# Optimization experiments

Measured on AMD Instinct MI355X. Metric: run time of the kernel, lower is better.

## Reference

```python
import jax, jax.numpy as jnp
import numpy as np

# Inner-product factors for Cl(1,3) (Minkowski metric diag(+,-,-,-)).
# For blade e_b, <~e_b e_b>_0 = product of the metric signs of its constituent vectors.
# Blade order: [1, e0,e1,e2,e3, e01,e02,e03,e12,e13,e23, e012,e013,e023,e123, e0123]
_IPF = jnp.array([1, 1, -1, -1, -1, -1, -1, -1, 1, 1, 1, 1, 1, 1, -1, -1], dtype=jnp.float32)

B, H, N, CMV, CS = 4, 8, 2048, 8, 16


def setup_inputs() -> dict:
    key = jax.random.key(0)
    ks = jax.random.split(key, 6)
    f = lambda k, s: jax.random.normal(k, s, dtype=jnp.float32)
    return {
        "q_mv": f(ks[0], (B, H, N, CMV, 16)),
        "k_mv": f(ks[1], (B, H, N, CMV, 16)),
        "v_mv": f(ks[2], (B, H, N, CMV, 16)),
        "q_s": f(ks[3], (B, H, N, CS)),
        "k_s": f(ks[4], (B, H, N, CS)),
        "v_s": f(ks[5], (B, H, N, CS)),
    }


def reference(q_mv, k_mv, v_mv, q_s, k_s, v_s):
    b, h, n, cmv, _ = q_mv.shape
    cs = q_s.shape[-1]
    cmv_out = v_mv.shape[-2]
    cs_out = v_s.shape[-1]
    # GA inner product on mv part = euclidean dot after applying metric factors to queries
    q = jnp.concatenate([(q_mv * _IPF).reshape(b, h, n, cmv * 16), q_s], axis=-1)
    k = jnp.concatenate([k_mv.reshape(b, h, n, cmv * 16), k_s], axis=-1)
    v = jnp.concatenate([v_mv.reshape(b, h, n, cmv_out * 16), v_s], axis=-1)
    scale = 1.0 / np.sqrt(q.shape[-1]).astype(np.float32)  # torch SDPA default scale
    scores = jnp.einsum("bhid,bhjd->bhij", q, k) * scale  # [B,H,N,N]
    attn = jax.nn.softmax(scores, axis=-1)
    out = jnp.einsum("bhij,bhjd->bhid", attn, v)
    out_mv = out[..., : cmv_out * 16].reshape(b, h, n, cmv_out, 16)
    out_s = out[..., cmv_out * 16 : cmv_out * 16 + cs_out]
    return out_mv, out_s
```

## Files before the change

### kernel.cpp

```cpp
#include <hip/hip_runtime.h>
#include <cstdint>
#include <math.h>


#define BH    32
#define N_    2048
#define DMV   128
#define DS    16
#define D_    144
#define BM    128
#define BN    64
#define NKIT  (N_ / BN)
#define KSTR  168
#define VSTR  72
#define PSTR  72
#define KP_BYTES  ((size_t)BH * N_ * KSTR * 2)
#define QSCALE 0.12022458674074693f

typedef __bf16 bf16_8 __attribute__((ext_vector_type(8)));
typedef __bf16 bf16_4 __attribute__((ext_vector_type(4)));
typedef __bf16 bf16_2 __attribute__((ext_vector_type(2)));
typedef float  f32x4  __attribute__((ext_vector_type(4)));

#define GLOAD_LDS16(g, l)                                                     \
  __builtin_amdgcn_global_load_lds(                                           \
      (const __attribute__((address_space(1))) void*)(g),                     \
      (__attribute__((address_space(3))) void*)(l), 16, 0, 0)

__device__ __forceinline__ f32x4 mfma16(bf16_8 a, bf16_8 b, f32x4 c) {
  return __builtin_amdgcn_mfma_f32_16x16x32_bf16(a, b, c, 0, 0, 0);
}

__device__ __forceinline__ bf16_4 cvt4(f32x4 x) {
  bf16_4 w; w[0]=(__bf16)x[0]; w[1]=(__bf16)x[1]; w[2]=(__bf16)x[2]; w[3]=(__bf16)x[3];
  return w;
}

__global__ __launch_bounds__(256)
void pack_k(const float* __restrict__ kmv, const float* __restrict__ ks_,
            __bf16* __restrict__ kp) {
  const unsigned g = blockIdx.x * 256 + threadIdx.x;
  const unsigned row = g / 21u, seg = g - row * 21u;
  bf16_8 o;
  if (seg < 16) {
    const f32x4* p = (const f32x4*)(kmv + (size_t)row * DMV + seg * 8);
    f32x4 a = p[0], b = p[1];
#pragma unroll
    for (int j = 0; j < 8; ++j) o[j] = (__bf16)((j < 4) ? a[j] : b[j - 4]);
  } else if (seg < 18) {
    const f32x4* p = (const f32x4*)(ks_ + (size_t)row * DS + (seg - 16) * 8);
    f32x4 a = p[0], b = p[1];
#pragma unroll
    for (int j = 0; j < 8; ++j) o[j] = (__bf16)((j < 4) ? a[j] : b[j - 4]);
  } else {
#pragma unroll
    for (int j = 0; j < 8; ++j) o[j] = (__bf16)0.0f;
  }
  *(bf16_8*)(kp + (size_t)row * KSTR + seg * 8) = o;
}

#define TSTR 156
__global__ __launch_bounds__(256)
void pack_vt(const float* __restrict__ vmv, const float* __restrict__ vs,
             __bf16* __restrict__ vt) {
  __shared__ __bf16 sT[64 * TSTR];
  const int tile = blockIdx.x;
  const int t = threadIdx.x;
  const int n = t >> 2, c = t & 3;
  const float* mv = vmv + (size_t)(tile * 64 + n) * DMV;
  const float* s  = vs  + (size_t)(tile * 64 + n) * DS;
  __bf16* row = &sT[n * TSTR];
  if (c < 3) {
#pragma unroll
    for (int i = 0; i < 9; ++i)
      *(bf16_4*)&row[c * 36 + 4 * i] = cvt4(*(const f32x4*)(mv + c * 36 + 4 * i));
  } else {
#pragma unroll
    for (int i = 0; i < 5; ++i)
      *(bf16_4*)&row[108 + 4 * i] = cvt4(*(const f32x4*)(mv + 108 + 4 * i));
#pragma unroll
    for (int i = 0; i < 4; ++i)
      *(bf16_4*)&row[128 + 4 * i] = cvt4(*(const f32x4*)(s + 4 * i));
  }
  __syncthreads();
  __bf16* vtt = vt + (size_t)tile * (D_ * VSTR);
#pragma unroll
  for (int k = 0; k < 18; ++k) {
    int idx = t + 256 * k;
    int d = idx >> 5, j = idx & 31;
    bf16_2 p; p[0] = sT[(2 * j) * TSTR + d]; p[1] = sT[(2 * j + 1) * TSTR + d];
    *(bf16_2*)&vtt[d * VSTR + 2 * j] = p;
  }
}

__device__ __forceinline__ bf16_8 load_q_frag(const float* qmv_row, const float* qs_row, int k0) {
  bf16_8 f;
  if (k0 < DMV) {
    const f32x4* p = (const f32x4*)(qmv_row + k0);
    f32x4 a = p[0], b = p[1];
    int hi = k0 & 8;
#pragma unroll
    for (int j = 0; j < 8; ++j) {
      float v = (j < 4) ? a[j] : b[j - 4];
      bool pos = hi ? (j < 6) : (j < 2);
      f[j] = (__bf16)(v * (pos ? QSCALE : -QSCALE));
    }
  } else if (k0 < D_) {
    const f32x4* p = (const f32x4*)(qs_row + (k0 - DMV));
    f32x4 a = p[0], b = p[1];
#pragma unroll
    for (int j = 0; j < 8; ++j) {
      float v = (j < 4) ? a[j] : b[j - 4];
      f[j] = (__bf16)(v * QSCALE);
    }
  } else {
#pragma unroll
    for (int j = 0; j < 8; ++j) f[j] = (__bf16)0.0f;
  }
  return f;
}

__global__ __launch_bounds__(512, 4)
void geo_attn_kernel(const float* __restrict__ q_mv, const float* __restrict__ q_s,
                     const __bf16* __restrict__ kp, const __bf16* __restrict__ vt,
                     float* __restrict__ out)
{
  __shared__ __bf16 sK[BN * KSTR];
  __shared__ __bf16 sVT[D_ * VSTR];

  const int tid  = threadIdx.x;
  const int w    = tid >> 6;
  const int lane = tid & 63;
  const int l15  = lane & 15;
  const int quad = lane >> 4;
  const int bh    = blockIdx.y;
  const int qbase = blockIdx.x * BM;
  const size_t bh_n = (size_t)bh * N_;

  __bf16* sP = sK + w * (16 * PSTR);

  bf16_8 qf[5];
  {
    int mrow = qbase + 16 * w + l15;
    const float* qmv_row = q_mv + (bh_n + mrow) * DMV;
    const float* qs_row  = q_s  + (bh_n + mrow) * DS;
#pragma unroll
    for (int ks = 0; ks < 5; ++ks)
      qf[ks] = load_q_frag(qmv_row, qs_row, ks * 32 + quad * 8);
  }

  f32x4 of[9];
#pragma unroll
  for (int n9 = 0; n9 < 9; ++n9)
#pragma unroll
    for (int r = 0; r < 4; ++r) of[n9][r] = 0.0f;
  float m_i = -INFINITY, l_i = 0.0f;

  const __bf16* kbase = kp + bh_n * KSTR;

  for (int it = 0; it < NKIT; ++it) {
    {
      const __bf16* kt  = kbase + (size_t)(it * BN) * KSTR;
      const __bf16* vtt = vt + (size_t)(bh * NKIT + it) * (D_ * VSTR);
      for (int i = w; i < 21; i += 8)
        GLOAD_LDS16(kt + i * 512 + lane * 8, &sK[i * 512 + lane * 8]);
      for (int i = w; i < 20; i += 8)
        GLOAD_LDS16(vtt + i * 512 + lane * 8, &sVT[i * 512 + lane * 8]);
      if (w == 0 && lane < 16)
        GLOAD_LDS16(vtt + 20 * 512 + lane * 8, &sVT[20 * 512 + lane * 8]);
    }
    __syncthreads();

    f32x4 sf[4];
#pragma unroll
    for (int nt = 0; nt < 4; ++nt)
#pragma unroll
      for (int r = 0; r < 4; ++r) sf[nt][r] = 0.0f;
#pragma unroll
    for (int ks = 0; ks < 5; ++ks) {
#pragma unroll
      for (int nt = 0; nt < 4; ++nt) {
        bf16_8 kb = *(const bf16_8*)&sK[(nt * 16 + l15) * KSTR + ks * 32 + quad * 8];
        sf[nt] = mfma16(kb, qf[ks], sf[nt]);
      }
    }
    __syncthreads();

    {
      float mx = sf[0][0];
#pragma unroll
      for (int nt = 0; nt < 4; ++nt)
#pragma unroll
        for (int r = 0; r < 4; ++r) mx = fmaxf(mx, sf[nt][r]);
      mx = fmaxf(mx, __shfl_xor(mx, 16));
      mx = fmaxf(mx, __shfl_xor(mx, 32));
      float mnew = fmaxf(m_i, mx);
      float al = __builtin_amdgcn_exp2f(m_i - mnew);
      m_i = mnew;
      float rs = 0.0f;
#pragma unroll
      for (int nt = 0; nt < 4; ++nt)
#pragma unroll
        for (int r = 0; r < 4; ++r) {
          float p = __builtin_amdgcn_exp2f(sf[nt][r] - mnew);
          sf[nt][r] = p;
          rs += p;
        }
      rs += __shfl_xor(rs, 16);
      rs += __shfl_xor(rs, 32);
      l_i = l_i * al + rs;

#pragma unroll
      for (int nt = 0; nt < 4; ++nt) {
        bf16_4 pw;
#pragma unroll
        for (int r = 0; r < 4; ++r) pw[r] = (__bf16)sf[nt][r];
        *(bf16_4*)&sP[l15 * PSTR + nt * 16 + quad * 4] = pw;
      }
      asm volatile("s_waitcnt lgkmcnt(0)" ::: "memory");

      float alr[4];
#pragma unroll
      for (int r = 0; r < 4; ++r) alr[r] = __shfl(al, 20 * quad + r);
#pragma unroll
      for (int n9 = 0; n9 < 9; ++n9)
#pragma unroll
        for (int r = 0; r < 4; ++r) of[n9][r] *= alr[r];
    }

#pragma unroll
    for (int ks = 0; ks < 2; ++ks) {
      bf16_8 pa = *(const bf16_8*)&sP[l15 * PSTR + ks * 32 + quad * 8];
#pragma unroll
      for (int n9 = 0; n9 < 9; ++n9) {
        bf16_8 vb = *(const bf16_8*)&sVT[(n9 * 16 + l15) * VSTR + ks * 32 + quad * 8];
        of[n9] = mfma16(pa, vb, of[n9]);
      }
    }
    __syncthreads();
  }

  float* out_mv = out;
  float* out_s  = out + (size_t)BH * N_ * DMV;
  float linv[4];
#pragma unroll
  for (int r = 0; r < 4; ++r)
    linv[r] = __builtin_amdgcn_rcpf(__shfl(l_i, 20 * quad + r));
#pragma unroll
  for (int n9 = 0; n9 < 9; ++n9) {
#pragma unroll
    for (int r = 0; r < 4; ++r) {
      int row = qbase + 16 * w + quad * 4 + r;
      float val = of[n9][r] * linv[r];
      if (n9 < 8) out_mv[(bh_n + row) * DMV + n9 * 16 + l15] = val;
      else        out_s [(bh_n + row) * DS + l15] = val;
    }
  }
}

extern "C" void kernel_launch(void* const* d_in, const int* in_sizes, int n_in,
                              void* d_out, int out_size, void* d_ws, size_t ws_size,
                              hipStream_t stream) {
  (void)in_sizes; (void)n_in; (void)out_size; (void)ws_size;
  const float* q_mv = (const float*)d_in[0];
  const float* k_mv = (const float*)d_in[1];
  const float* v_mv = (const float*)d_in[2];
  const float* q_s  = (const float*)d_in[3];
  const float* k_s  = (const float*)d_in[4];
  const float* v_s  = (const float*)d_in[5];
  float* out = (float*)d_out;

  __bf16* kp = (__bf16*)d_ws;
  __bf16* vt = (__bf16*)((char*)d_ws + KP_BYTES);

  pack_k<<<(BH * N_ * 21) / 256, 256, 0, stream>>>(k_mv, k_s, kp);
  pack_vt<<<BH * NKIT, 256, 0, stream>>>(v_mv, v_s, vt);

  dim3 grid(N_ / BM, BH);
  geo_attn_kernel<<<grid, 512, 0, stream>>>(q_mv, q_s, kp, vt, out);
}
```

Measured before the change: 273.6 us.

## Pre-swizzle K/V tiles into MFMA fragment order and give each wave two row groups

The pack kernels now write K and V^T tiles in the exact per-lane MFMA fragment order, so LDS reads become contiguous lane*8 accesses with no padding strides. The attention kernel drops from 8 waves to 4 per block, and each wave handles 32 query rows as two 16-row groups. Every K and V fragment loaded from LDS is then reused for two MFMAs. This cuts LDS traffic and bank conflicts per MFMA, but it doubles accumulator registers per wave and lowers wave count per block, which may hurt occupancy and latency hiding.

```diff
diff --git a/kernel.cpp b/kernel.cpp
--- a/kernel.cpp
+++ b/kernel.cpp
@@ -11,15 +11,13 @@
 #define BM    128
 #define BN    64
 #define NKIT  (N_ / BN)
-#define KSTR  168
-#define VSTR  72
 #define PSTR  72
-#define KP_BYTES  ((size_t)BH * N_ * KSTR * 2)
+#define KTILE_E  10240
+#define VTILE_E  9216
+#define KP_BYTES ((size_t)BH * NKIT * KTILE_E * 2)
 #define QSCALE 0.12022458674074693f
 
 typedef __bf16 bf16_8 __attribute__((ext_vector_type(8)));
-typedef __bf16 bf16_4 __attribute__((ext_vector_type(4)));
-typedef __bf16 bf16_2 __attribute__((ext_vector_type(2)));
 typedef float  f32x4  __attribute__((ext_vector_type(4)));
 
 #define GLOAD_LDS16(g, l)                                                     \
@@ -31,32 +29,37 @@
   return __builtin_amdgcn_mfma_f32_16x16x32_bf16(a, b, c, 0, 0, 0);
 }
 
-__device__ __forceinline__ bf16_4 cvt4(f32x4 x) {
-  bf16_4 w; w[0]=(__bf16)x[0]; w[1]=(__bf16)x[1]; w[2]=(__bf16)x[2]; w[3]=(__bf16)x[3];
-  return w;
-}
-
 __global__ __launch_bounds__(256)
 void pack_k(const float* __restrict__ kmv, const float* __restrict__ ks_,
             __bf16* __restrict__ kp) {
-  const unsigned g = blockIdx.x * 256 + threadIdx.x;
-  const unsigned row = g / 21u, seg = g - row * 21u;
-  bf16_8 o;
-  if (seg < 16) {
-    const f32x4* p = (const f32x4*)(kmv + (size_t)row * DMV + seg * 8);
-    f32x4 a = p[0], b = p[1];
-#pragma unroll
-    for (int j = 0; j < 8; ++j) o[j] = (__bf16)((j < 4) ? a[j] : b[j - 4]);
-  } else if (seg < 18) {
-    const f32x4* p = (const f32x4*)(ks_ + (size_t)row * DS + (seg - 16) * 8);
-    f32x4 a = p[0], b = p[1];
-#pragma unroll
-    for (int j = 0; j < 8; ++j) o[j] = (__bf16)((j < 4) ? a[j] : b[j - 4]);
-  } else {
-#pragma unroll
-    for (int j = 0; j < 8; ++j) o[j] = (__bf16)0.0f;
-  }
-  *(bf16_8*)(kp + (size_t)row * KSTR + seg * 8) = o;
+  const int tile = blockIdx.x;
+  const int t = threadIdx.x;
+  __bf16* dst = kp + (size_t)tile * KTILE_E;
+#pragma unroll
+  for (int u = 0; u < 5; ++u) {
+    int c = t + 256 * u;
+    int f = c >> 6, r = c & 63;
+    int nt = f / 5, ks = f - nt * 5;
+    int quad = r >> 4, l15 = r & 15;
+    int n = tile * 64 + nt * 16 + l15;
+    int k = ks * 32 + quad * 8;
+    bf16_8 o;
+    if (k < DMV) {
+      const f32x4* p = (const f32x4*)(kmv + (size_t)n * DMV + k);
+      f32x4 a = p[0], b = p[1];
+#pragma unroll
+      for (int j = 0; j < 8; ++j) o[j] = (__bf16)((j < 4) ? a[j] : b[j - 4]);
+    } else if (k < D_) {
+      const f32x4* p = (const f32x4*)(ks_ + (size_t)n * DS + (k - DMV));
+      f32x4 a = p[0], b = p[1];
+#pragma unroll
+      for (int j = 0; j < 8; ++j) o[j] = (__bf16)((j < 4) ? a[j] : b[j - 4]);
+    } else {
+#pragma unroll
+      for (int j = 0; j < 8; ++j) o[j] = (__bf16)0.0f;
+    }
+    *(bf16_8*)(dst + (size_t)c * 8) = o;
+  }
 }
 
 #define TSTR 156
@@ -66,30 +69,45 @@
   __shared__ __bf16 sT[64 * TSTR];
   const int tile = blockIdx.x;
   const int t = threadIdx.x;
-  const int n = t >> 2, c = t & 3;
-  const float* mv = vmv + (size_t)(tile * 64 + n) * DMV;
-  const float* s  = vs  + (size_t)(tile * 64 + n) * DS;
-  __bf16* row = &sT[n * TSTR];
-  if (c < 3) {
-#pragma unroll
-    for (int i = 0; i < 9; ++i)
-      *(bf16_4*)&row[c * 36 + 4 * i] = cvt4(*(const f32x4*)(mv + c * 36 + 4 * i));
-  } else {
-#pragma unroll
-    for (int i = 0; i < 5; ++i)
-      *(bf16_4*)&row[108 + 4 * i] = cvt4(*(const f32x4*)(mv + 108 + 4 * i));
-#pragma unroll
-    for (int i = 0; i < 4; ++i)
-      *(bf16_4*)&row[128 + 4 * i] = cvt4(*(const f32x4*)(s + 4 * i));
+  {
+    const int n = t >> 2, c4 = t & 3;
+    const float* mv = vmv + (size_t)(tile * 64 + n) * DMV;
+    const float* s  = vs  + (size_t)(tile * 64 + n) * DS;
+    __bf16* row = &sT[n * TSTR];
+    if (c4 < 3) {
+#pragma unroll
+      for (int i = 0; i < 9; ++i) {
+        f32x4 x = *(const f32x4*)(mv + c4 * 36 + 4 * i);
+#pragma unroll
+        for (int j = 0; j < 4; ++j) row[c4 * 36 + 4 * i + j] = (__bf16)x[j];
+      }
+    } else {
+#pragma unroll
+      for (int i = 0; i < 5; ++i) {
+        f32x4 x = *(const f32x4*)(mv + 108 + 4 * i);
+#pragma unroll
+        for (int j = 0; j < 4; ++j) row[108 + 4 * i + j] = (__bf16)x[j];
+      }
+#pragma unroll
+      for (int i = 0; i < 4; ++i) {
+        f32x4 x = *(const f32x4*)(s + 4 * i);
+#pragma unroll
+        for (int j = 0; j < 4; ++j) row[128 + 4 * i + j] = (__bf16)x[j];
+      }
+    }
   }
   __syncthreads();
-  __bf16* vtt = vt + (size_t)tile * (D_ * VSTR);
-#pragma unroll
-  for (int k = 0; k < 18; ++k) {
-    int idx = t + 256 * k;
-    int d = idx >> 5, j = idx & 31;
-    bf16_2 p; p[0] = sT[(2 * j) * TSTR + d]; p[1] = sT[(2 * j + 1) * TSTR + d];
-    *(bf16_2*)&vtt[d * VSTR + 2 * j] = p;
+  __bf16* dst = vt + (size_t)tile * VTILE_E;
+  for (int c = t; c < 1152; c += 256) {
+    int f = c >> 6, r = c & 63;
+    int n9 = f >> 1, ks = f & 1;
+    int quad = r >> 4, l15 = r & 15;
+    int d = n9 * 16 + l15;
+    int n0 = ks * 32 + quad * 8;
+    bf16_8 o;
+#pragma unroll
+    for (int j = 0; j < 8; ++j) o[j] = sT[(n0 + j) * TSTR + d];
+    *(bf16_8*)(dst + (size_t)c * 8) = o;
   }
 }
 
@@ -120,13 +138,13 @@
   return f;
 }
 
-__global__ __launch_bounds__(512, 4)
+__global__ __launch_bounds__(256, 3)
 void geo_attn_kernel(const float* __restrict__ q_mv, const float* __restrict__ q_s,
                      const __bf16* __restrict__ kp, const __bf16* __restrict__ vt,
                      float* __restrict__ out)
 {
-  __shared__ __bf16 sK[BN * KSTR];
-  __shared__ __bf16 sVT[D_ * VSTR];
+  __shared__ __bf16 sK[KTILE_E];
+  __shared__ __bf16 sVT[VTILE_E];
 
   const int tid  = threadIdx.x;
   const int w    = tid >> 6;
@@ -137,87 +155,92 @@
   const int qbase = blockIdx.x * BM;
   const size_t bh_n = (size_t)bh * N_;
 
-  __bf16* sP = sK + w * (16 * PSTR);
-
-  bf16_8 qf[5];
-  {
-    int mrow = qbase + 16 * w + l15;
+  __bf16* sPw = sK + w * (32 * PSTR);
+
+  bf16_8 qf[2][5];
+#pragma unroll
+  for (int rg = 0; rg < 2; ++rg) {
+    int mrow = qbase + 32 * w + 16 * rg + l15;
     const float* qmv_row = q_mv + (bh_n + mrow) * DMV;
     const float* qs_row  = q_s  + (bh_n + mrow) * DS;
 #pragma unroll
     for (int ks = 0; ks < 5; ++ks)
-      qf[ks] = load_q_frag(qmv_row, qs_row, ks * 32 + quad * 8);
-  }
-
-  f32x4 of[9];
-#pragma unroll
-  for (int n9 = 0; n9 < 9; ++n9)
-#pragma unroll
-    for (int r = 0; r < 4; ++r) of[n9][r] = 0.0f;
-  float m_i = -INFINITY, l_i = 0.0f;
-
-  const __bf16* kbase = kp + bh_n * KSTR;
+      qf[rg][ks] = load_q_frag(qmv_row, qs_row, ks * 32 + quad * 8);
+  }
+
+  f32x4 of[2][9];
+#pragma unroll
+  for (int rg = 0; rg < 2; ++rg)
+#pragma unroll
+    for (int n9 = 0; n9 < 9; ++n9)
+#pragma unroll
+      for (int r = 0; r < 4; ++r) of[rg][n9][r] = 0.0f;
+  float m_i[2] = {-INFINITY, -INFINITY}, l_i[2] = {0.0f, 0.0f};
+
+  const __bf16* kbase = kp + (size_t)bh * NKIT * KTILE_E;
+  const __bf16* vbase = vt + (size_t)bh * NKIT * VTILE_E;
 
   for (int it = 0; it < NKIT; ++it) {
     {
-      const __bf16* kt  = kbase + (size_t)(it * BN) * KSTR;
-      const __bf16* vtt = vt + (size_t)(bh * NKIT + it) * (D_ * VSTR);
-      for (int i = w; i < 21; i += 8)
+      const __bf16* kt = kbase + (size_t)it * KTILE_E;
+      const __bf16* vp = vbase + (size_t)it * VTILE_E;
+      for (int i = w; i < 20; i += 4)
         GLOAD_LDS16(kt + i * 512 + lane * 8, &sK[i * 512 + lane * 8]);
-      for (int i = w; i < 20; i += 8)
-        GLOAD_LDS16(vtt + i * 512 + lane * 8, &sVT[i * 512 + lane * 8]);
-      if (w == 0 && lane < 16)
-        GLOAD_LDS16(vtt + 20 * 512 + lane * 8, &sVT[20 * 512 + lane * 8]);
+      for (int i = w; i < 18; i += 4)
+        GLOAD_LDS16(vp + i * 512 + lane * 8, &sVT[i * 512 + lane * 8]);
     }
     __syncthreads();
 
-    f32x4 sf[4];
-#pragma unroll
-    for (int nt = 0; nt < 4; ++nt)
-#pragma unroll
-      for (int r = 0; r < 4; ++r) sf[nt][r] = 0.0f;
+    f32x4 sf[2][4];
+#pragma unroll
+    for (int rg = 0; rg < 2; ++rg)
+#pragma unroll
+      for (int nt = 0; nt < 4; ++nt)
+#pragma unroll
+        for (int r = 0; r < 4; ++r) sf[rg][nt][r] = 0.0f;
 #pragma unroll
     for (int ks = 0; ks < 5; ++ks) {
 #pragma unroll
       for (int nt = 0; nt < 4; ++nt) {
-        bf16_8 kb = *(const bf16_8*)&sK[(nt * 16 + l15) * KSTR + ks * 32 + quad * 8];
-        sf[nt] = mfma16(kb, qf[ks], sf[nt]);
+        bf16_8 kb = *(const bf16_8*)&sK[(nt * 5 + ks) * 512 + lane * 8];
+        sf[0][nt] = mfma16(kb, qf[0][ks], sf[0][nt]);
+        sf[1][nt] = mfma16(kb, qf[1][ks], sf[1][nt]);
       }
     }
     __syncthreads();
 
-    {
-      float mx = sf[0][0];
+#pragma unroll
+    for (int rg = 0; rg < 2; ++rg) {
+      float mx = sf[rg][0][0];
 #pragma unroll
       for (int nt = 0; nt < 4; ++nt)
 #pragma unroll
-        for (int r = 0; r < 4; ++r) mx = fmaxf(mx, sf[nt][r]);
+        for (int r = 0; r < 4; ++r) mx = fmaxf(mx, sf[rg][nt][r]);
       mx = fmaxf(mx, __shfl_xor(mx, 16));
       mx = fmaxf(mx, __shfl_xor(mx, 32));
-      float mnew = fmaxf(m_i, mx);
-      float al = __builtin_amdgcn_exp2f(m_i - mnew);
-      m_i = mnew;
+      float mnew = fmaxf(m_i[rg], mx);
+      float al = __builtin_amdgcn_exp2f(m_i[rg] - mnew);
+      m_i[rg] = mnew;
       float rs = 0.0f;
 #pragma unroll
       for (int nt = 0; nt < 4; ++nt)
 #pragma unroll
         for (int r = 0; r < 4; ++r) {
-          float p = __builtin_amdgcn_exp2f(sf[nt][r] - mnew);
-          sf[nt][r] = p;
+          float p = __builtin_amdgcn_exp2f(sf[rg][nt][r] - mnew);
+          sf[rg][nt][r] = p;
           rs += p;
         }
       rs += __shfl_xor(rs, 16);
       rs += __shfl_xor(rs, 32);
-      l_i = l_i * al + rs;
+      l_i[rg] = l_i[rg] * al + rs;
 
 #pragma unroll
       for (int nt = 0; nt < 4; ++nt) {
-        bf16_4 pw;
-#pragma unroll
-        for (int r = 0; r < 4; ++r) pw[r] = (__bf16)sf[nt][r];
-        *(bf16_4*)&sP[l15 * PSTR + nt * 16 + quad * 4] = pw;
-      }
-      asm volatile("s_waitcnt lgkmcnt(0)" ::: "memory");
+        __bf16 pw[4];
+#pragma unroll
+        for (int r = 0; r < 4; ++r) pw[r] = (__bf16)sf[rg][nt][r];
+        *(uint64_t*)&sPw[(rg * 16 + l15) * PSTR + nt * 16 + quad * 4] = *(uint64_t*)pw;
+      }
 
       float alr[4];
 #pragma unroll
@@ -225,16 +248,21 @@
 #pragma unroll
       for (int n9 = 0; n9 < 9; ++n9)
 #pragma unroll
-        for (int r = 0; r < 4; ++r) of[n9][r] *= alr[r];
-    }
+        for (int r = 0; r < 4; ++r) of[rg][n9][r] *= alr[r];
+    }
+    asm volatile("s_waitcnt lgkmcnt(0)" ::: "memory");
 
 #pragma unroll
     for (int ks = 0; ks < 2; ++ks) {
-      bf16_8 pa = *(const bf16_8*)&sP[l15 * PSTR + ks * 32 + quad * 8];
+      bf16_8 pa[2];
+#pragma unroll
+      for (int rg = 0; rg < 2; ++rg)
+        pa[rg] = *(const bf16_8*)&sPw[(rg * 16 + l15) * PSTR + ks * 32 + quad * 8];
 #pragma unroll
       for (int n9 = 0; n9 < 9; ++n9) {
-        bf16_8 vb = *(const bf16_8*)&sVT[(n9 * 16 + l15) * VSTR + ks * 32 + quad * 8];
-        of[n9] = mfma16(pa, vb, of[n9]);
+        bf16_8 vb = *(const bf16_8*)&sVT[(n9 * 2 + ks) * 512 + lane * 8];
+        of[0][n9] = mfma16(pa[0], vb, of[0][n9]);
+        of[1][n9] = mfma16(pa[1], vb, of[1][n9]);
       }
     }
     __syncthreads();
@@ -242,18 +270,21 @@
 
   float* out_mv = out;
   float* out_s  = out + (size_t)BH * N_ * DMV;
-  float linv[4];
-#pragma unroll
-  for (int r = 0; r < 4; ++r)
-    linv[r] = __builtin_amdgcn_rcpf(__shfl(l_i, 20 * quad + r));
-#pragma unroll
-  for (int n9 = 0; n9 < 9; ++n9) {
-#pragma unroll
-    for (int r = 0; r < 4; ++r) {
-      int row = qbase + 16 * w + quad * 4 + r;
-      float val = of[n9][r] * linv[r];
-      if (n9 < 8) out_mv[(bh_n + row) * DMV + n9 * 16 + l15] = val;
-      else        out_s [(bh_n + row) * DS + l15] = val;
+#pragma unroll
+  for (int rg = 0; rg < 2; ++rg) {
+    float linv[4];
+#pragma unroll
+    for (int r = 0; r < 4; ++r)
+      linv[r] = __builtin_amdgcn_rcpf(__shfl(l_i[rg], 20 * quad + r));
+#pragma unroll
+    for (int n9 = 0; n9 < 9; ++n9) {
+#pragma unroll
+      for (int r = 0; r < 4; ++r) {
+        int row = qbase + 32 * w + 16 * rg + quad * 4 + r;
+        float val = of[rg][n9][r] * linv[r];
+        if (n9 < 8) out_mv[(bh_n + row) * DMV + n9 * 16 + l15] = val;
+        else        out_s [(bh_n + row) * DS + l15] = val;
+      }
     }
   }
 }
@@ -273,9 +304,9 @@
   __bf16* kp = (__bf16*)d_ws;
   __bf16* vt = (__bf16*)((char*)d_ws + KP_BYTES);
 
-  pack_k<<<(BH * N_ * 21) / 256, 256, 0, stream>>>(k_mv, k_s, kp);
+  pack_k<<<BH * NKIT, 256, 0, stream>>>(k_mv, k_s, kp);
   pack_vt<<<BH * NKIT, 256, 0, stream>>>(v_mv, v_s, vt);
 
   dim3 grid(N_ / BM, BH);
-  geo_attn_kernel<<<grid, 512, 0, stream>>>(q_mv, q_s, kp, vt, out);
-}
+  geo_attn_kernel<<<grid, 256, 0, stream>>>(q_mv, q_s, kp, vt, out);
+}
```

New measurement: 296.5 us. 8.4% more time.
